# Kernel tuning notes

Hardware: AMD Instinct MI355X
Metric: run time of the kernel (lower is better)

Reference implementation:

```python
import jax, jax.numpy as jnp
import numpy as np

DIM = 1024
NUM_HEAD = 8
INNER = DIM // NUM_HEAD
B, L = 2, 2048
EPS = 1e-5  # GroupNorm default eps


def _xavier(key, out_d, in_d, gain=0.01):
    std = gain * np.sqrt(2.0 / (in_d + out_d))
    return (jax.random.normal(key, (out_d, in_d), jnp.float32) * std)


def setup_inputs() -> dict:
    key = jax.random.key(0)
    ks = jax.random.split(key, 12)
    x = jax.random.normal(ks[0], (B, L, DIM), jnp.float32)
    hidden = jax.random.normal(ks[1], (B, NUM_HEAD, INNER), jnp.float32)
    # dt bias: inv-softplus of dt ~ LogUniform(0.001, 0.1), as in __init__
    dt = jnp.exp(jax.random.uniform(ks[2], (NUM_HEAD,), jnp.float32,
                                    minval=np.log(0.001), maxval=np.log(0.1)))
    b_dt = dt + jnp.log1p(-jnp.exp(-dt))
    ln_a = jnp.log(jax.random.uniform(ks[3], (NUM_HEAD,), jnp.float32, minval=1.0, maxval=16.0))
    return {
        "x": x, "hidden": hidden,
        "W_z": _xavier(ks[4], DIM, DIM), "b_z": jnp.zeros((DIM,), jnp.float32),
        "W_z_act": _xavier(ks[5], DIM, DIM), "b_z_act": jnp.zeros((DIM,), jnp.float32),
        "W_y": _xavier(ks[6], DIM, DIM), "b_y": jnp.zeros((DIM,), jnp.float32),
        "W_y_act": _xavier(ks[7], DIM, DIM), "b_y_act": jnp.zeros((DIM,), jnp.float32),
        "W_dt": _xavier(ks[8], NUM_HEAD, DIM), "b_dt": b_dt,
        "ln_a": ln_a,
        "gn_w": jnp.ones((NUM_HEAD,), jnp.float32), "gn_b": jnp.zeros((NUM_HEAD,), jnp.float32),
    }


def reference(x, hidden, W_z, b_z, W_z_act, b_z_act, W_y, b_y, W_y_act, b_y_act,
              W_dt, b_dt, ln_a, gn_w, gn_b):
    b, l, d = x.shape
    nh, inner = NUM_HEAD, d // NUM_HEAD
    silu = jax.nn.silu
    xf = x.astype(jnp.float32)
    # gated input projection -> z: [b,l,h,i]
    z = ((xf @ W_z.T + b_z) * silu(xf @ W_z_act.T + b_z_act)).reshape(b, l, nh, inner)
    # log-decay per step: [b,l,h]
    ln_da = -jnp.exp(ln_a) * jax.nn.softplus(xf @ W_dt.T + b_dt)
    # einops.repeat 'b l h -> b l m h' then torch .tril(-1) (masks over LAST TWO dims (m,h))
    ln_da_masked = jnp.tril(jnp.broadcast_to(ln_da[:, :, None, :], (b, l, l, nh)), k=-1)
    # rfft/irfft conv with ones == prefix sum along l (dim 1)
    ln_da_masked_conv = jnp.cumsum(ln_da_masked, axis=1)
    da_masked_conv = jnp.tril(jnp.exp(ln_da_masked_conv))  # tril over (m,h), k=0
    h_inner = jnp.einsum('blmh,bmhi->blhi', da_masked_conv, z)
    # cross-chunk: cumulative decay applied to carried hidden state
    da_cum = jnp.exp(jnp.cumsum(ln_da, axis=1))  # [b,l,h]
    h_cross = jnp.einsum('blh,bhi->blhi', da_cum, hidden)
    h = h_inner + h_cross  # [b,l,h,i]
    hidden_next = h[:, -1]
    # GroupNorm(num_head groups, num_head channels) on [b*l, h, i]:
    # one channel per group -> normalize over inner dim per (token, head)
    mean = h.mean(axis=-1, keepdims=True)
    var = h.var(axis=-1, keepdims=True)
    h_norm = (h - mean) / jnp.sqrt(var + EPS) * gn_w[None, None, :, None] + gn_b[None, None, :, None]
    h_norm = h_norm.reshape(b, l, d)
    y = (h_norm @ W_y.T + b_y) * silu(xf @ W_y_act.T + b_y_act)
    return y.astype(x.dtype), hidden_next
```

## Files before the change

kernel.cpp:

```cpp
#include <hip/hip_runtime.h>
#include <stdint.h>

#define DIM   1024
#define L_SEQ 2048
#define BATCH 2
#define NH    8
#define M_TOT 4096
#define EPS_F 1e-5f

typedef __bf16 bf16x8 __attribute__((ext_vector_type(8)));
typedef unsigned short u16x8 __attribute__((ext_vector_type(8)));
typedef float f32x4 __attribute__((ext_vector_type(4)));

__device__ __forceinline__ unsigned short f2bf(float f) {
  unsigned int u = __float_as_uint(f);
  u += 0x7FFFu + ((u >> 16) & 1u);
  return (unsigned short)(u >> 16);
}

__device__ __forceinline__ f32x4 mfma_bf16(u16x8 a, u16x8 b, f32x4 c) {
  return __builtin_amdgcn_mfma_f32_16x16x32_bf16(
      __builtin_bit_cast(bf16x8, a), __builtin_bit_cast(bf16x8, b), c, 0, 0, 0);
}

__device__ __forceinline__ float silu_f(float v) {
  return v / (1.f + __expf(-v));
}

__device__ __forceinline__ void gload16(const unsigned short* g, unsigned short* l) {
  __builtin_amdgcn_global_load_lds(
      (const __attribute__((address_space(1))) unsigned int*)g,
      (__attribute__((address_space(3))) unsigned int*)l, 16, 0, 0);
}

__global__ __launch_bounds__(256) void prep_kernel(const float* __restrict__ x,
                                                   const float* __restrict__ W_dt,
                                                   const float* __restrict__ b_dt,
                                                   const float* __restrict__ ln_a,
                                                   const float4* __restrict__ wz,
                                                   const float4* __restrict__ wza,
                                                   const float4* __restrict__ wya,
                                                   float* __restrict__ ln_da,
                                                   unsigned short* __restrict__ xb,
                                                   ushort4* __restrict__ wzb,
                                                   ushort4* __restrict__ wzab,
                                                   ushort4* __restrict__ wyab,
                                                   float* __restrict__ Zs) {
  const int blk = blockIdx.x;
  const int tid = threadIdx.x;
  if (blk >= 4096) {
    const int wb = blk - 4096;
    if (wb < 2) ((f32x4*)Zs)[wb * 256 + tid] = f32x4{0.f, 0.f, 0.f, 0.f};
    int i = wb * 256 + tid;
    const float4* s; ushort4* d; int j;
    if (i < 262144)      { s = wz;  d = wzb;  j = i; }
    else if (i < 524288) { s = wza; d = wzab; j = i - 262144; }
    else                 { s = wya; d = wyab; j = i - 524288; }
    float4 f = s[j];
    d[j] = make_ushort4(f2bf(f.x), f2bf(f.y), f2bf(f.z), f2bf(f.w));
    return;
  }
  __shared__ float partials[NH][4];
  const int row = blk;
  const int wave = tid >> 6, lane = tid & 63;
  float4 f = ((const float4*)(x + (size_t)row * DIM))[tid];
  ((ushort4*)(xb + (size_t)row * DIM))[tid] =
      make_ushort4(f2bf(f.x), f2bf(f.y), f2bf(f.z), f2bf(f.w));
#pragma unroll
  for (int h = 0; h < NH; ++h) {
    const float4 w = ((const float4*)(W_dt + (size_t)h * DIM))[tid];
    float p = f.x * w.x + f.y * w.y + f.z * w.z + f.w * w.w;
    for (int off = 32; off > 0; off >>= 1) p += __shfl_down(p, off);
    if (lane == 0) partials[h][wave] = p;
  }
  __syncthreads();
  if (tid < 32) {
    const int h = tid >> 2, wv = tid & 3;
    float s = partials[h][wv];
    s += __shfl_down(s, 1);
    s += __shfl_down(s, 2);
    if (wv == 0) {
      float t = s + b_dt[h];
      float sp = (t > 20.f) ? t : log1pf(expf(t));
      int b = row >> 11, l = row & (L_SEQ - 1);
      ln_da[(size_t)(b * NH + h) * L_SEQ + l] = -expf(ln_a[h]) * sp;
    }
  }
}

__global__ __launch_bounds__(256, 4) void gemm_all(const unsigned short* __restrict__ xb,
                                                   const unsigned short* __restrict__ Wz,
                                                   const unsigned short* __restrict__ Wza,
                                                   const unsigned short* __restrict__ Wya,
                                                   const float* __restrict__ b_z,
                                                   const float* __restrict__ b_za,
                                                   const float* __restrict__ b_ya,
                                                   float* __restrict__ Zs,
                                                   float* __restrict__ wdiag,
                                                   float* __restrict__ Sy) {
  __shared__ __align__(16) unsigned short As[128 * 64];
  __shared__ __align__(16) unsigned short Bs[128 * 64];
  __shared__ float colsum[64];

  const int tid = threadIdx.x;
  const int lane = tid & 63, wave = tid >> 6;
  const int wm = wave >> 1, wn = wave & 1;
  const int l16 = lane & 15, quad = lane >> 4;

  const int flat = blockIdx.x;
  const int xcd = flat & 7;
  const int j = flat >> 3;
  const int nt = 3 * xcd + (j % 3);
  const int mt = j / 3;
  const bool isZ = (nt < 16);
  const int n0 = isZ ? nt * 64 : (nt - 16) * 128;
  const int m0 = mt * 128;

  const int rowl = tid >> 3;
  const int g = (tid & 7) ^ (rowl & 7);
  const size_t aoff = (size_t)(m0 + rowl) * DIM + g * 8;
  const size_t boff = (size_t)(n0 + rowl) * DIM + g * 8;
  const unsigned short* bp0 = isZ ? Wz : Wya;
  const unsigned short* bp1 = isZ ? Wza : (Wya + (size_t)64 * DIM);
  unsigned short* AsD = As + tid * 8;
  unsigned short* BsD = Bs + tid * 8;

  f32x4 acc[4][4];
  const f32x4 zero = {0.f, 0.f, 0.f, 0.f};
  for (int i = 0; i < 4; ++i)
    for (int jj = 0; jj < 4; ++jj) acc[i][jj] = zero;

  for (int kt = 0; kt < 16; ++kt) {
    const size_t k0 = (size_t)kt * 64;
    __syncthreads();
    gload16(xb  + aoff + k0,                AsD);
    gload16(xb  + aoff + 32 * DIM + k0,     AsD + 2048);
    gload16(xb  + aoff + 64 * DIM + k0,     AsD + 4096);
    gload16(xb  + aoff + 96 * DIM + k0,     AsD + 6144);
    gload16(bp0 + boff + k0,                BsD);
    gload16(bp0 + boff + 32 * DIM + k0,     BsD + 2048);
    gload16(bp1 + boff + k0,                BsD + 4096);
    gload16(bp1 + boff + 32 * DIM + k0,     BsD + 6144);
    __syncthreads();
#pragma unroll
    for (int kk = 0; kk < 2; ++kk) {
      const int kc = kk * 4 + quad;
      u16x8 aF[4], bF[4];
#pragma unroll
      for (int rb = 0; rb < 4; ++rb) {
        const int r = wm * 64 + rb * 16 + l16;
        aF[rb] = *(const u16x8*)&As[r * 64 + ((kc ^ (r & 7)) << 3)];
      }
#pragma unroll
      for (int cb = 0; cb < 4; ++cb) {
        int r;
        if (isZ) r = (cb < 2) ? (wn * 32 + cb * 16 + l16)
                              : (64 + wn * 32 + (cb - 2) * 16 + l16);
        else     r = wn * 64 + cb * 16 + l16;
        bF[cb] = *(const u16x8*)&Bs[r * 64 + ((kc ^ (r & 7)) << 3)];
      }
#pragma unroll
      for (int rb = 0; rb < 4; ++rb)
#pragma unroll
        for (int cb = 0; cb < 4; ++cb)
          acc[rb][cb] = mfma_bf16(aF[rb], bF[cb], acc[rb][cb]);
    }
  }

  if (isZ) {
    __syncthreads();
    if (tid < 64) colsum[tid] = 0.f;
    __syncthreads();
    const int b = m0 >> 11;
#pragma unroll
    for (int cb = 0; cb < 2; ++cb) {
      const int nl = wn * 32 + cb * 16 + l16;
      const int n = n0 + nl;
      const int h = n >> 7;
      const float bz = b_z[n], ba = b_za[n];
      float ssum = 0.f;
#pragma unroll
      for (int rb = 0; rb < 4; ++rb) {
        const int mlb = wm * 64 + rb * 16 + quad * 4;
#pragma unroll
        for (int r = 0; r < 4; ++r) {
          const int l = (m0 + mlb + r) & (L_SEQ - 1);
          float u  = acc[rb][cb][r] + bz;
          float vv = acc[rb][cb + 2][r] + ba;
          if (l > h) ssum += u * silu_f(vv);
          else if (l == h)
            wdiag[(size_t)(b * NH + h) * 128 + (n & 127)] = u * silu_f(vv);
        }
      }
      atomicAdd(&colsum[nl], ssum);
    }
    __syncthreads();
    if (tid < 64) atomicAdd(&Zs[(size_t)b * DIM + n0 + tid], colsum[tid]);
  } else {
#pragma unroll
    for (int cb = 0; cb < 4; ++cb) {
      const int nl = wn * 64 + cb * 16 + l16;
      const float bb = b_ya[n0 + nl];
#pragma unroll
      for (int rb = 0; rb < 4; ++rb) {
        const int mlb = wm * 64 + rb * 16 + quad * 4;
#pragma unroll
        for (int r = 0; r < 4; ++r)
          Sy[(size_t)(m0 + mlb + r) * DIM + n0 + nl] = silu_f(acc[rb][cb][r] + bb);
      }
    }
  }
}

__global__ __launch_bounds__(256) void stats_scan(const float* __restrict__ Zs,
                                                  const float* __restrict__ hidden,
                                                  const float* __restrict__ wdiag,
                                                  const float* __restrict__ gn_w,
                                                  const float* __restrict__ ln_da,
                                                  float* __restrict__ vtg,
                                                  float* __restrict__ wtg,
                                                  float* __restrict__ alpha2,
                                                  float* __restrict__ hidden_next) {
  const int bh = blockIdx.x, b = bh >> 3, h = bh & 7;
  const int tid = threadIdx.x, wv = tid >> 6, lane = tid & 63;
  __shared__ float csumS[32];
  __shared__ float statS[4];

  float v0 = 0.f, v1 = 0.f, w0 = 0.f, w1 = 0.f;
  const size_t base = (size_t)bh * 128;
  if (wv == 0) {
    v0 = Zs[(size_t)b * DIM + h * 128 + lane]      + hidden[base + lane];
    v1 = Zs[(size_t)b * DIM + h * 128 + 64 + lane] + hidden[base + 64 + lane];
    w0 = wdiag[base + lane];
    w1 = wdiag[base + 64 + lane];
    float sv = v0 + v1, sw = w0 + w1;
    for (int off = 32; off > 0; off >>= 1) {
      sv += __shfl_down(sv, off);
      sw += __shfl_down(sw, off);
    }
    const float muv = __shfl(sv, 0) * (1.f / 128.f);
    const float muw = __shfl(sw, 0) * (1.f / 128.f);
    const float a0 = v0 - muv, a1 = v1 - muv;
    const float c0 = w0 - muw, c1 = w1 - muw;
    float rvv = a0 * a0 + a1 * a1;
    float rvw = a0 * c0 + a1 * c1;
    float rww = c0 * c0 + c1 * c1;
    for (int off = 32; off > 0; off >>= 1) {
      rvv += __shfl_down(rvv, off);
      rvw += __shfl_down(rvw, off);
      rww += __shfl_down(rww, off);
    }
    if (lane == 0) {
      statS[0] = rvv * (1.f / 128.f);
      statS[1] = rvw * (1.f / 128.f);
      statS[2] = rww * (1.f / 128.f);
    }
    const float gw = gn_w[h];
    vtg[base + lane] = a0 * gw;  vtg[base + 64 + lane] = a1 * gw;
    wtg[base + lane] = c0 * gw;  wtg[base + 64 + lane] = c1 * gw;
  }

  const float* src = ln_da + (size_t)bh * L_SEQ;
  float vals[8];
#pragma unroll
  for (int jj = 0; jj < 8; ++jj) {
    const int c = wv * 8 + jj;
    float val = src[c * 64 + lane];
#pragma unroll
    for (int off = 1; off < 64; off <<= 1) {
      float nv = __shfl_up(val, off);
      if (lane >= off) val += nv;
    }
    vals[jj] = val;
    if (lane == 63) csumS[c] = val;
  }
  __syncthreads();

  if (tid < 32) {
    float s = csumS[tid];
    float incl = s;
#pragma unroll
    for (int off = 1; off < 32; off <<= 1) {
      float nv = __shfl_up(incl, off);
      if (tid >= off) incl += nv;
    }
    csumS[tid] = incl - s;
    if (tid == 31) statS[3] = incl;
  }
  __syncthreads();

  const float svv = statS[0], svw = statS[1], sww = statS[2];
#pragma unroll
  for (int jj = 0; jj < 8; ++jj) {
    const int c = wv * 8 + jj;
    const float S = csumS[c] + vals[jj];
    const float ce = expf(S);
    const float D = rsqrtf(ce * ce * svv + 2.f * ce * svw + sww + EPS_F);
    const int l = c * 64 + lane;
    float* ap = alpha2 + ((size_t)(b * L_SEQ + l) * NH + h) * 2;
    ap[0] = ce * D;
    ap[1] = D;
  }
  if (wv == 0) {
    const float clast = expf(statS[3]);
    hidden_next[base + lane]      = clast * v0 + w0;
    hidden_next[base + 64 + lane] = clast * v1 + w1;
  }
}

__global__ __launch_bounds__(256) void proj_kernel(const float* __restrict__ W_y,
                                                   const float* __restrict__ vtg,
                                                   const float* __restrict__ wtg,
                                                   const float* __restrict__ gn_b,
                                                   const float* __restrict__ b_y,
                                                   float* __restrict__ Gv,
                                                   float* __restrict__ Gw,
                                                   float* __restrict__ constc) {
  const int tid = threadIdx.x, wave = tid >> 6, lane = tid & 63;
  const int n = blockIdx.x * 4 + wave;
  const float4* row = (const float4*)(W_y + (size_t)n * DIM);
  const int half = lane >> 5, l32 = lane & 31;
  float cc = 0.f;
#pragma unroll
  for (int p = 0; p < 4; ++p) {
    const int h = p * 2 + half;
    float4 wv = row[p * 64 + lane];
    const float4 va = *(const float4*)&vtg[(size_t)h * 128 + l32 * 4];
    const float4 vb = *(const float4*)&vtg[(size_t)(8 + h) * 128 + l32 * 4];
    const float4 wa = *(const float4*)&wtg[(size_t)h * 128 + l32 * 4];
    const float4 wb = *(const float4*)&wtg[(size_t)(8 + h) * 128 + l32 * 4];
    float gv0 = wv.x * va.x + wv.y * va.y + wv.z * va.z + wv.w * va.w;
    float gv1 = wv.x * vb.x + wv.y * vb.y + wv.z * vb.z + wv.w * vb.w;
    float gw0 = wv.x * wa.x + wv.y * wa.y + wv.z * wa.z + wv.w * wa.w;
    float gw1 = wv.x * wb.x + wv.y * wb.y + wv.z * wb.z + wv.w * wb.w;
    cc += (wv.x + wv.y + wv.z + wv.w) * gn_b[h];
#pragma unroll
    for (int off = 16; off > 0; off >>= 1) {
      gv0 += __shfl_down(gv0, off, 32);
      gv1 += __shfl_down(gv1, off, 32);
      gw0 += __shfl_down(gw0, off, 32);
      gw1 += __shfl_down(gw1, off, 32);
    }
    if (l32 == 0) {
      Gv[(size_t)h * DIM + n]       = gv0;
      Gv[(size_t)(8 + h) * DIM + n] = gv1;
      Gw[(size_t)h * DIM + n]       = gw0;
      Gw[(size_t)(8 + h) * DIM + n] = gw1;
    }
  }
  for (int off = 32; off > 0; off >>= 1) cc += __shfl_down(cc, off);
  if (lane == 0) constc[n] = b_y[n] + cc;
}

__global__ __launch_bounds__(256) void finalize(const float* __restrict__ alpha2,
                                                const float* __restrict__ Gv,
                                                const float* __restrict__ Gw,
                                                const float* __restrict__ constc,
                                                float* __restrict__ y) {
  const int tid = threadIdx.x;
  const int n0 = blockIdx.x * 256;
  const int m0 = blockIdx.y * 64;
  const int b = m0 >> 11;
  __shared__ float aS[64 * 16];
  ((float4*)aS)[tid] = ((const float4*)(alpha2 + (size_t)m0 * 16))[tid];
  __syncthreads();
  const int c = tid & 63;
  const int rg = tid >> 6;
  const int n = n0 + c * 4;
  f32x4 g[16 * 2];
#pragma unroll
  for (int h = 0; h < 8; ++h) {
    g[2 * h]     = *(const f32x4*)&Gv[(size_t)(b * NH + h) * DIM + n];
    g[2 * h + 1] = *(const f32x4*)&Gw[(size_t)(b * NH + h) * DIM + n];
  }
  const f32x4 cc = *(const f32x4*)&constc[n];
#pragma unroll
  for (int jj = 0; jj < 16; ++jj) {
    const int m = m0 + rg * 16 + jj;
    const float* a = &aS[(rg * 16 + jj) * 16];
    f32x4 Ay = cc;
#pragma unroll
    for (int k = 0; k < 16; ++k) Ay += a[k] * g[k];
    f32x4 s = *(const f32x4*)&y[(size_t)m * DIM + n];
    *(f32x4*)&y[(size_t)m * DIM + n] = Ay * s;
  }
}

extern "C" void kernel_launch(void* const* d_in, const int* in_sizes, int n_in,
                              void* d_out, int out_size, void* d_ws, size_t ws_size,
                              hipStream_t stream) {
  const float* x      = (const float*)d_in[0];
  const float* hidden = (const float*)d_in[1];
  const float* W_z    = (const float*)d_in[2];
  const float* b_z    = (const float*)d_in[3];
  const float* W_za   = (const float*)d_in[4];
  const float* b_za   = (const float*)d_in[5];
  const float* W_y    = (const float*)d_in[6];
  const float* b_y    = (const float*)d_in[7];
  const float* W_ya   = (const float*)d_in[8];
  const float* b_ya   = (const float*)d_in[9];
  const float* W_dt   = (const float*)d_in[10];
  const float* b_dt   = (const float*)d_in[11];
  const float* ln_a   = (const float*)d_in[12];
  const float* gn_w   = (const float*)d_in[13];
  const float* gn_b   = (const float*)d_in[14];

  char* ws = (char*)d_ws;
  unsigned short* xb   = (unsigned short*)(ws);
  unsigned short* Wzb  = (unsigned short*)(ws + 8388608);
  unsigned short* Wzab = (unsigned short*)(ws + 10485760);
  unsigned short* Wyab = (unsigned short*)(ws + 12582912);
  float* ln_da  = (float*)(ws + 14680064);
  float* Zs     = (float*)(ws + 14811136);
  float* wdiag  = (float*)(ws + 14819328);
  float* vtg    = (float*)(ws + 14827520);
  float* wtg    = (float*)(ws + 14835712);
  float* Gv     = (float*)(ws + 14843904);
  float* Gw     = (float*)(ws + 14909440);
  float* constc = (float*)(ws + 14974976);
  float* alpha2 = (float*)(ws + 14979072);

  float* y = (float*)d_out;
  float* hidden_next = y + (size_t)M_TOT * DIM;

  prep_kernel<<<7168, 256, 0, stream>>>(x, W_dt, b_dt, ln_a,
                                        (const float4*)W_z, (const float4*)W_za,
                                        (const float4*)W_ya,
                                        ln_da, xb, (ushort4*)Wzb, (ushort4*)Wzab,
                                        (ushort4*)Wyab, Zs);

  gemm_all<<<768, 256, 0, stream>>>(xb, Wzb, Wzab, Wyab,
                                    b_z, b_za, b_ya, Zs, wdiag, y);

  stats_scan<<<16, 256, 0, stream>>>(Zs, hidden, wdiag, gn_w, ln_da,
                                     vtg, wtg, alpha2, hidden_next);
  proj_kernel<<<256, 256, 0, stream>>>(W_y, vtg, wtg, gn_b, b_y, Gv, Gw, constc);

  finalize<<<dim3(4, 64), 256, 0, stream>>>(alpha2, Gv, Gw, constc, y);
}
```

Before: 165.0 us.

## Merge five kernel launches into two persistent kernels with grid barriers

```diff
diff --git a/kernel.cpp b/kernel.cpp
--- a/kernel.cpp
+++ b/kernel.cpp
@@ -33,356 +33,387 @@
       (__attribute__((address_space(3))) unsigned int*)l, 16, 0, 0);
 }
 
-__global__ __launch_bounds__(256) void prep_kernel(const float* __restrict__ x,
-                                                   const float* __restrict__ W_dt,
-                                                   const float* __restrict__ b_dt,
-                                                   const float* __restrict__ ln_a,
-                                                   const float4* __restrict__ wz,
-                                                   const float4* __restrict__ wza,
-                                                   const float4* __restrict__ wya,
-                                                   float* __restrict__ ln_da,
-                                                   unsigned short* __restrict__ xb,
-                                                   ushort4* __restrict__ wzb,
-                                                   ushort4* __restrict__ wzab,
-                                                   ushort4* __restrict__ wyab,
-                                                   float* __restrict__ Zs) {
-  const int blk = blockIdx.x;
-  const int tid = threadIdx.x;
-  if (blk >= 4096) {
-    const int wb = blk - 4096;
-    if (wb < 2) ((f32x4*)Zs)[wb * 256 + tid] = f32x4{0.f, 0.f, 0.f, 0.f};
-    int i = wb * 256 + tid;
-    const float4* s; ushort4* d; int j;
-    if (i < 262144)      { s = wz;  d = wzb;  j = i; }
-    else if (i < 524288) { s = wza; d = wzab; j = i - 262144; }
-    else                 { s = wya; d = wyab; j = i - 524288; }
-    float4 f = s[j];
-    d[j] = make_ushort4(f2bf(f.x), f2bf(f.y), f2bf(f.z), f2bf(f.w));
-    return;
-  }
-  __shared__ float partials[NH][4];
-  const int row = blk;
-  const int wave = tid >> 6, lane = tid & 63;
-  float4 f = ((const float4*)(x + (size_t)row * DIM))[tid];
-  ((ushort4*)(xb + (size_t)row * DIM))[tid] =
-      make_ushort4(f2bf(f.x), f2bf(f.y), f2bf(f.z), f2bf(f.w));
-#pragma unroll
-  for (int h = 0; h < NH; ++h) {
-    const float4 w = ((const float4*)(W_dt + (size_t)h * DIM))[tid];
-    float p = f.x * w.x + f.y * w.y + f.z * w.z + f.w * w.w;
-    for (int off = 32; off > 0; off >>= 1) p += __shfl_down(p, off);
-    if (lane == 0) partials[h][wave] = p;
-  }
+
+__device__ __forceinline__ void grid_bar(unsigned int* cnt, unsigned int target) {
   __syncthreads();
-  if (tid < 32) {
-    const int h = tid >> 2, wv = tid & 3;
-    float s = partials[h][wv];
-    s += __shfl_down(s, 1);
-    s += __shfl_down(s, 2);
-    if (wv == 0) {
-      float t = s + b_dt[h];
-      float sp = (t > 20.f) ? t : log1pf(expf(t));
-      int b = row >> 11, l = row & (L_SEQ - 1);
-      ln_da[(size_t)(b * NH + h) * L_SEQ + l] = -expf(ln_a[h]) * sp;
-    }
-  }
-}
-
-__global__ __launch_bounds__(256, 4) void gemm_all(const unsigned short* __restrict__ xb,
-                                                   const unsigned short* __restrict__ Wz,
-                                                   const unsigned short* __restrict__ Wza,
-                                                   const unsigned short* __restrict__ Wya,
-                                                   const float* __restrict__ b_z,
-                                                   const float* __restrict__ b_za,
-                                                   const float* __restrict__ b_ya,
-                                                   float* __restrict__ Zs,
-                                                   float* __restrict__ wdiag,
-                                                   float* __restrict__ Sy) {
+  if (threadIdx.x == 0) {
+    __threadfence();
+    __hip_atomic_fetch_add(cnt, 1u, __ATOMIC_RELAXED, __HIP_MEMORY_SCOPE_AGENT);
+    while (__hip_atomic_load(cnt, __ATOMIC_RELAXED, __HIP_MEMORY_SCOPE_AGENT) < target) {
+      __builtin_amdgcn_s_sleep(8);
+    }
+    __threadfence();
+  }
+  __syncthreads();
+}
+
+__global__ __launch_bounds__(256, 4) void coop_main(
+    const float*  __restrict__ x,
+    const float*  __restrict__ W_dt,
+    const float*  __restrict__ b_dt,
+    const float*  __restrict__ ln_a,
+    const float4* __restrict__ wz4,
+    const float4* __restrict__ wza4,
+    const float4* __restrict__ wya4,
+    float*        __restrict__ ln_da,
+    unsigned short* __restrict__ xb,
+    float*        __restrict__ Zs,
+    const float*  __restrict__ b_z,
+    const float*  __restrict__ b_za,
+    const float*  __restrict__ b_ya,
+    float*        __restrict__ wdiag,
+    float*        __restrict__ y,
+    unsigned short* __restrict__ Wzb,
+    unsigned short* __restrict__ Wzab,
+    unsigned short* __restrict__ Wyab,
+    unsigned int*  __restrict__ bars) {
   __shared__ __align__(16) unsigned short As[128 * 64];
   __shared__ __align__(16) unsigned short Bs[128 * 64];
   __shared__ float colsum[64];
+  __shared__ float partials[NH][4];
 
   const int tid = threadIdx.x;
+  const int blk = blockIdx.x;
   const int lane = tid & 63, wave = tid >> 6;
-  const int wm = wave >> 1, wn = wave & 1;
-  const int l16 = lane & 15, quad = lane >> 4;
-
-  const int flat = blockIdx.x;
-  const int xcd = flat & 7;
-  const int j = flat >> 3;
-  const int nt = 3 * xcd + (j % 3);
-  const int mt = j / 3;
-  const bool isZ = (nt < 16);
-  const int n0 = isZ ? nt * 64 : (nt - 16) * 128;
-  const int m0 = mt * 128;
-
-  const int rowl = tid >> 3;
-  const int g = (tid & 7) ^ (rowl & 7);
-  const size_t aoff = (size_t)(m0 + rowl) * DIM + g * 8;
-  const size_t boff = (size_t)(n0 + rowl) * DIM + g * 8;
-  const unsigned short* bp0 = isZ ? Wz : Wya;
-  const unsigned short* bp1 = isZ ? Wza : (Wya + (size_t)64 * DIM);
-  unsigned short* AsD = As + tid * 8;
-  unsigned short* BsD = Bs + tid * 8;
-
-  f32x4 acc[4][4];
-  const f32x4 zero = {0.f, 0.f, 0.f, 0.f};
-  for (int i = 0; i < 4; ++i)
-    for (int jj = 0; jj < 4; ++jj) acc[i][jj] = zero;
-
-  for (int kt = 0; kt < 16; ++kt) {
-    const size_t k0 = (size_t)kt * 64;
-    __syncthreads();
-    gload16(xb  + aoff + k0,                AsD);
-    gload16(xb  + aoff + 32 * DIM + k0,     AsD + 2048);
-    gload16(xb  + aoff + 64 * DIM + k0,     AsD + 4096);
-    gload16(xb  + aoff + 96 * DIM + k0,     AsD + 6144);
-    gload16(bp0 + boff + k0,                BsD);
-    gload16(bp0 + boff + 32 * DIM + k0,     BsD + 2048);
-    gload16(bp1 + boff + k0,                BsD + 4096);
-    gload16(bp1 + boff + 32 * DIM + k0,     BsD + 6144);
-    __syncthreads();
-#pragma unroll
-    for (int kk = 0; kk < 2; ++kk) {
-      const int kc = kk * 4 + quad;
-      u16x8 aF[4], bF[4];
-#pragma unroll
-      for (int rb = 0; rb < 4; ++rb) {
-        const int r = wm * 64 + rb * 16 + l16;
-        aF[rb] = *(const u16x8*)&As[r * 64 + ((kc ^ (r & 7)) << 3)];
-      }
+
+  {
+    ushort4* wzb4  = (ushort4*)Wzb;
+    ushort4* wzab4 = (ushort4*)Wzab;
+    ushort4* wyab4 = (ushort4*)Wyab;
+#pragma unroll
+    for (int it = 0; it < 4; ++it) {
+      const int i = it * 196608 + blk * 256 + tid;
+      const float4* s; ushort4* d; int j;
+      if (i < 262144)      { s = wz4;  d = wzb4;  j = i; }
+      else if (i < 524288) { s = wza4; d = wzab4; j = i - 262144; }
+      else                 { s = wya4; d = wyab4; j = i - 524288; }
+      float4 f = s[j];
+      d[j] = make_ushort4(f2bf(f.x), f2bf(f.y), f2bf(f.z), f2bf(f.w));
+    }
+    if (blk == 0) {
+      ((f32x4*)Zs)[tid]       = f32x4{0.f, 0.f, 0.f, 0.f};
+      ((f32x4*)Zs)[tid + 256] = f32x4{0.f, 0.f, 0.f, 0.f};
+    }
+    for (int it = 0; it < 6; ++it) {
+      const int row = it * 768 + blk;
+      if (row < 4096) {
+        float4 f = ((const float4*)(x + (size_t)row * DIM))[tid];
+        ((ushort4*)(xb + (size_t)row * DIM))[tid] =
+            make_ushort4(f2bf(f.x), f2bf(f.y), f2bf(f.z), f2bf(f.w));
+#pragma unroll
+        for (int h = 0; h < NH; ++h) {
+          const float4 w = ((const float4*)(W_dt + (size_t)h * DIM))[tid];
+          float p = f.x * w.x + f.y * w.y + f.z * w.z + f.w * w.w;
+          for (int off = 32; off > 0; off >>= 1) p += __shfl_down(p, off);
+          if (lane == 0) partials[h][wave] = p;
+        }
+        __syncthreads();
+        if (tid < 32) {
+          const int h = tid >> 2, wv = tid & 3;
+          float s = partials[h][wv];
+          s += __shfl_down(s, 1);
+          s += __shfl_down(s, 2);
+          if (wv == 0) {
+            float t = s + b_dt[h];
+            float sp = (t > 20.f) ? t : log1pf(expf(t));
+            int b = row >> 11, l = row & (L_SEQ - 1);
+            ln_da[(size_t)(b * NH + h) * L_SEQ + l] = -expf(ln_a[h]) * sp;
+          }
+        }
+        __syncthreads();
+      }
+    }
+  }
+
+  grid_bar(bars + 0, 768u);
+
+  {
+    const int wm = wave >> 1, wn = wave & 1;
+    const int l16 = lane & 15, quad = lane >> 4;
+
+    const int flat = blk;
+    const int xcd = flat & 7;
+    const int j = flat >> 3;
+    const int nt = 3 * xcd + (j % 3);
+    const int mt = j / 3;
+    const bool isZ = (nt < 16);
+    const int n0 = isZ ? nt * 64 : (nt - 16) * 128;
+    const int m0 = mt * 128;
+
+    const int rowl = tid >> 3;
+    const int g = (tid & 7) ^ (rowl & 7);
+    const size_t aoff = (size_t)(m0 + rowl) * DIM + g * 8;
+    const size_t boff = (size_t)(n0 + rowl) * DIM + g * 8;
+    const unsigned short* bp0 = isZ ? Wzb : Wyab;
+    const unsigned short* bp1 = isZ ? Wzab : (Wyab + (size_t)64 * DIM);
+    unsigned short* AsD = As + tid * 8;
+    unsigned short* BsD = Bs + tid * 8;
+
+    f32x4 acc[4][4];
+    const f32x4 zero = {0.f, 0.f, 0.f, 0.f};
+    for (int i = 0; i < 4; ++i)
+      for (int jj = 0; jj < 4; ++jj) acc[i][jj] = zero;
+
+    for (int kt = 0; kt < 16; ++kt) {
+      const size_t k0 = (size_t)kt * 64;
+      __syncthreads();
+      gload16(xb  + aoff + k0,                AsD);
+      gload16(xb  + aoff + 32 * DIM + k0,     AsD + 2048);
+      gload16(xb  + aoff + 64 * DIM + k0,     AsD + 4096);
+      gload16(xb  + aoff + 96 * DIM + k0,     AsD + 6144);
+      gload16(bp0 + boff + k0,                BsD);
+      gload16(bp0 + boff + 32 * DIM + k0,     BsD + 2048);
+      gload16(bp1 + boff + k0,                BsD + 4096);
+      gload16(bp1 + boff + 32 * DIM + k0,     BsD + 6144);
+      __syncthreads();
+#pragma unroll
+      for (int kk = 0; kk < 2; ++kk) {
+        const int kc = kk * 4 + quad;
+        u16x8 aF[4], bF[4];
+#pragma unroll
+        for (int rb = 0; rb < 4; ++rb) {
+          const int r = wm * 64 + rb * 16 + l16;
+          aF[rb] = *(const u16x8*)&As[r * 64 + ((kc ^ (r & 7)) << 3)];
+        }
+#pragma unroll
+        for (int cb = 0; cb < 4; ++cb) {
+          int r;
+          if (isZ) r = (cb < 2) ? (wn * 32 + cb * 16 + l16)
+                                : (64 + wn * 32 + (cb - 2) * 16 + l16);
+          else     r = wn * 64 + cb * 16 + l16;
+          bF[cb] = *(const u16x8*)&Bs[r * 64 + ((kc ^ (r & 7)) << 3)];
+        }
+#pragma unroll
+        for (int rb = 0; rb < 4; ++rb)
+#pragma unroll
+          for (int cb = 0; cb < 4; ++cb)
+            acc[rb][cb] = mfma_bf16(aF[rb], bF[cb], acc[rb][cb]);
+      }
+    }
+
+    if (isZ) {
+      __syncthreads();
+      if (tid < 64) colsum[tid] = 0.f;
+      __syncthreads();
+      const int b = m0 >> 11;
+#pragma unroll
+      for (int cb = 0; cb < 2; ++cb) {
+        const int nl = wn * 32 + cb * 16 + l16;
+        const int n = n0 + nl;
+        const int h = n >> 7;
+        const float bz = b_z[n], ba = b_za[n];
+        float ssum = 0.f;
+#pragma unroll
+        for (int rb = 0; rb < 4; ++rb) {
+          const int mlb = wm * 64 + rb * 16 + quad * 4;
+#pragma unroll
+          for (int r = 0; r < 4; ++r) {
+            const int l = (m0 + mlb + r) & (L_SEQ - 1);
+            float u  = acc[rb][cb][r] + bz;
+            float vv = acc[rb][cb + 2][r] + ba;
+            if (l > h) ssum += u * silu_f(vv);
+            else if (l == h)
+              wdiag[(size_t)(b * NH + h) * 128 + (n & 127)] = u * silu_f(vv);
+          }
+        }
+        atomicAdd(&colsum[nl], ssum);
+      }
+      __syncthreads();
+      if (tid < 64) atomicAdd(&Zs[(size_t)b * DIM + n0 + tid], colsum[tid]);
+    } else {
 #pragma unroll
       for (int cb = 0; cb < 4; ++cb) {
-        int r;
-        if (isZ) r = (cb < 2) ? (wn * 32 + cb * 16 + l16)
-                              : (64 + wn * 32 + (cb - 2) * 16 + l16);
-        else     r = wn * 64 + cb * 16 + l16;
-        bF[cb] = *(const u16x8*)&Bs[r * 64 + ((kc ^ (r & 7)) << 3)];
-      }
-#pragma unroll
-      for (int rb = 0; rb < 4; ++rb)
-#pragma unroll
-        for (int cb = 0; cb < 4; ++cb)
-          acc[rb][cb] = mfma_bf16(aF[rb], bF[cb], acc[rb][cb]);
-    }
-  }
-
-  if (isZ) {
-    __syncthreads();
-    if (tid < 64) colsum[tid] = 0.f;
-    __syncthreads();
-    const int b = m0 >> 11;
-#pragma unroll
-    for (int cb = 0; cb < 2; ++cb) {
-      const int nl = wn * 32 + cb * 16 + l16;
-      const int n = n0 + nl;
-      const int h = n >> 7;
-      const float bz = b_z[n], ba = b_za[n];
-      float ssum = 0.f;
-#pragma unroll
-      for (int rb = 0; rb < 4; ++rb) {
-        const int mlb = wm * 64 + rb * 16 + quad * 4;
-#pragma unroll
-        for (int r = 0; r < 4; ++r) {
-          const int l = (m0 + mlb + r) & (L_SEQ - 1);
-          float u  = acc[rb][cb][r] + bz;
-          float vv = acc[rb][cb + 2][r] + ba;
-          if (l > h) ssum += u * silu_f(vv);
-          else if (l == h)
-            wdiag[(size_t)(b * NH + h) * 128 + (n & 127)] = u * silu_f(vv);
-        }
-      }
-      atomicAdd(&colsum[nl], ssum);
-    }
-    __syncthreads();
-    if (tid < 64) atomicAdd(&Zs[(size_t)b * DIM + n0 + tid], colsum[tid]);
-  } else {
-#pragma unroll
-    for (int cb = 0; cb < 4; ++cb) {
-      const int nl = wn * 64 + cb * 16 + l16;
-      const float bb = b_ya[n0 + nl];
-#pragma unroll
-      for (int rb = 0; rb < 4; ++rb) {
-        const int mlb = wm * 64 + rb * 16 + quad * 4;
-#pragma unroll
-        for (int r = 0; r < 4; ++r)
-          Sy[(size_t)(m0 + mlb + r) * DIM + n0 + nl] = silu_f(acc[rb][cb][r] + bb);
-      }
-    }
-  }
-}
-
-__global__ __launch_bounds__(256) void stats_scan(const float* __restrict__ Zs,
-                                                  const float* __restrict__ hidden,
-                                                  const float* __restrict__ wdiag,
-                                                  const float* __restrict__ gn_w,
-                                                  const float* __restrict__ ln_da,
-                                                  float* __restrict__ vtg,
-                                                  float* __restrict__ wtg,
-                                                  float* __restrict__ alpha2,
-                                                  float* __restrict__ hidden_next) {
-  const int bh = blockIdx.x, b = bh >> 3, h = bh & 7;
-  const int tid = threadIdx.x, wv = tid >> 6, lane = tid & 63;
+        const int nl = wn * 64 + cb * 16 + l16;
+        const float bb = b_ya[n0 + nl];
+#pragma unroll
+        for (int rb = 0; rb < 4; ++rb) {
+          const int mlb = wm * 64 + rb * 16 + quad * 4;
+#pragma unroll
+          for (int r = 0; r < 4; ++r)
+            y[(size_t)(m0 + mlb + r) * DIM + n0 + nl] = silu_f(acc[rb][cb][r] + bb);
+        }
+      }
+    }
+  }
+}
+
+__global__ __launch_bounds__(256) void coop_tail(
+    const float* __restrict__ Zs,
+    const float* __restrict__ hidden,
+    const float* __restrict__ wdiag,
+    const float* __restrict__ gn_w,
+    const float* __restrict__ ln_da,
+    float* __restrict__ vtg,
+    float* __restrict__ wtg,
+    float* __restrict__ alpha2,
+    float* __restrict__ hidden_next,
+    const float* __restrict__ W_y,
+    const float* __restrict__ gn_b,
+    const float* __restrict__ b_y,
+    float* __restrict__ Gv,
+    float* __restrict__ Gw,
+    float* __restrict__ constc,
+    float* __restrict__ y,
+    unsigned int* __restrict__ bars) {
+  const int tid = threadIdx.x;
+  const int blk = blockIdx.x;
   __shared__ float csumS[32];
   __shared__ float statS[4];
-
-  float v0 = 0.f, v1 = 0.f, w0 = 0.f, w1 = 0.f;
-  const size_t base = (size_t)bh * 128;
-  if (wv == 0) {
-    v0 = Zs[(size_t)b * DIM + h * 128 + lane]      + hidden[base + lane];
-    v1 = Zs[(size_t)b * DIM + h * 128 + 64 + lane] + hidden[base + 64 + lane];
-    w0 = wdiag[base + lane];
-    w1 = wdiag[base + 64 + lane];
-    float sv = v0 + v1, sw = w0 + w1;
-    for (int off = 32; off > 0; off >>= 1) {
-      sv += __shfl_down(sv, off);
-      sw += __shfl_down(sw, off);
-    }
-    const float muv = __shfl(sv, 0) * (1.f / 128.f);
-    const float muw = __shfl(sw, 0) * (1.f / 128.f);
-    const float a0 = v0 - muv, a1 = v1 - muv;
-    const float c0 = w0 - muw, c1 = w1 - muw;
-    float rvv = a0 * a0 + a1 * a1;
-    float rvw = a0 * c0 + a1 * c1;
-    float rww = c0 * c0 + c1 * c1;
-    for (int off = 32; off > 0; off >>= 1) {
-      rvv += __shfl_down(rvv, off);
-      rvw += __shfl_down(rvw, off);
-      rww += __shfl_down(rww, off);
-    }
-    if (lane == 0) {
-      statS[0] = rvv * (1.f / 128.f);
-      statS[1] = rvw * (1.f / 128.f);
-      statS[2] = rww * (1.f / 128.f);
-    }
-    const float gw = gn_w[h];
-    vtg[base + lane] = a0 * gw;  vtg[base + 64 + lane] = a1 * gw;
-    wtg[base + lane] = c0 * gw;  wtg[base + 64 + lane] = c1 * gw;
-  }
-
-  const float* src = ln_da + (size_t)bh * L_SEQ;
-  float vals[8];
-#pragma unroll
-  for (int jj = 0; jj < 8; ++jj) {
-    const int c = wv * 8 + jj;
-    float val = src[c * 64 + lane];
-#pragma unroll
-    for (int off = 1; off < 64; off <<= 1) {
-      float nv = __shfl_up(val, off);
-      if (lane >= off) val += nv;
-    }
-    vals[jj] = val;
-    if (lane == 63) csumS[c] = val;
-  }
-  __syncthreads();
-
-  if (tid < 32) {
-    float s = csumS[tid];
-    float incl = s;
-#pragma unroll
-    for (int off = 1; off < 32; off <<= 1) {
-      float nv = __shfl_up(incl, off);
-      if (tid >= off) incl += nv;
-    }
-    csumS[tid] = incl - s;
-    if (tid == 31) statS[3] = incl;
-  }
-  __syncthreads();
-
-  const float svv = statS[0], svw = statS[1], sww = statS[2];
-#pragma unroll
-  for (int jj = 0; jj < 8; ++jj) {
-    const int c = wv * 8 + jj;
-    const float S = csumS[c] + vals[jj];
-    const float ce = expf(S);
-    const float D = rsqrtf(ce * ce * svv + 2.f * ce * svw + sww + EPS_F);
-    const int l = c * 64 + lane;
-    float* ap = alpha2 + ((size_t)(b * L_SEQ + l) * NH + h) * 2;
-    ap[0] = ce * D;
-    ap[1] = D;
-  }
-  if (wv == 0) {
-    const float clast = expf(statS[3]);
-    hidden_next[base + lane]      = clast * v0 + w0;
-    hidden_next[base + 64 + lane] = clast * v1 + w1;
-  }
-}
-
-__global__ __launch_bounds__(256) void proj_kernel(const float* __restrict__ W_y,
-                                                   const float* __restrict__ vtg,
-                                                   const float* __restrict__ wtg,
-                                                   const float* __restrict__ gn_b,
-                                                   const float* __restrict__ b_y,
-                                                   float* __restrict__ Gv,
-                                                   float* __restrict__ Gw,
-                                                   float* __restrict__ constc) {
-  const int tid = threadIdx.x, wave = tid >> 6, lane = tid & 63;
-  const int n = blockIdx.x * 4 + wave;
-  const float4* row = (const float4*)(W_y + (size_t)n * DIM);
-  const int half = lane >> 5, l32 = lane & 31;
-  float cc = 0.f;
-#pragma unroll
-  for (int p = 0; p < 4; ++p) {
-    const int h = p * 2 + half;
-    float4 wv = row[p * 64 + lane];
-    const float4 va = *(const float4*)&vtg[(size_t)h * 128 + l32 * 4];
-    const float4 vb = *(const float4*)&vtg[(size_t)(8 + h) * 128 + l32 * 4];
-    const float4 wa = *(const float4*)&wtg[(size_t)h * 128 + l32 * 4];
-    const float4 wb = *(const float4*)&wtg[(size_t)(8 + h) * 128 + l32 * 4];
-    float gv0 = wv.x * va.x + wv.y * va.y + wv.z * va.z + wv.w * va.w;
-    float gv1 = wv.x * vb.x + wv.y * vb.y + wv.z * vb.z + wv.w * vb.w;
-    float gw0 = wv.x * wa.x + wv.y * wa.y + wv.z * wa.z + wv.w * wa.w;
-    float gw1 = wv.x * wb.x + wv.y * wb.y + wv.z * wb.z + wv.w * wb.w;
-    cc += (wv.x + wv.y + wv.z + wv.w) * gn_b[h];
-#pragma unroll
-    for (int off = 16; off > 0; off >>= 1) {
-      gv0 += __shfl_down(gv0, off, 32);
-      gv1 += __shfl_down(gv1, off, 32);
-      gw0 += __shfl_down(gw0, off, 32);
-      gw1 += __shfl_down(gw1, off, 32);
-    }
-    if (l32 == 0) {
-      Gv[(size_t)h * DIM + n]       = gv0;
-      Gv[(size_t)(8 + h) * DIM + n] = gv1;
-      Gw[(size_t)h * DIM + n]       = gw0;
-      Gw[(size_t)(8 + h) * DIM + n] = gw1;
-    }
-  }
-  for (int off = 32; off > 0; off >>= 1) cc += __shfl_down(cc, off);
-  if (lane == 0) constc[n] = b_y[n] + cc;
-}
-
-__global__ __launch_bounds__(256) void finalize(const float* __restrict__ alpha2,
-                                                const float* __restrict__ Gv,
-                                                const float* __restrict__ Gw,
-                                                const float* __restrict__ constc,
-                                                float* __restrict__ y) {
-  const int tid = threadIdx.x;
-  const int n0 = blockIdx.x * 256;
-  const int m0 = blockIdx.y * 64;
-  const int b = m0 >> 11;
   __shared__ float aS[64 * 16];
-  ((float4*)aS)[tid] = ((const float4*)(alpha2 + (size_t)m0 * 16))[tid];
-  __syncthreads();
-  const int c = tid & 63;
-  const int rg = tid >> 6;
-  const int n = n0 + c * 4;
-  f32x4 g[16 * 2];
-#pragma unroll
-  for (int h = 0; h < 8; ++h) {
-    g[2 * h]     = *(const f32x4*)&Gv[(size_t)(b * NH + h) * DIM + n];
-    g[2 * h + 1] = *(const f32x4*)&Gw[(size_t)(b * NH + h) * DIM + n];
-  }
-  const f32x4 cc = *(const f32x4*)&constc[n];
-#pragma unroll
-  for (int jj = 0; jj < 16; ++jj) {
-    const int m = m0 + rg * 16 + jj;
-    const float* a = &aS[(rg * 16 + jj) * 16];
-    f32x4 Ay = cc;
-#pragma unroll
-    for (int k = 0; k < 16; ++k) Ay += a[k] * g[k];
-    f32x4 s = *(const f32x4*)&y[(size_t)m * DIM + n];
-    *(f32x4*)&y[(size_t)m * DIM + n] = Ay * s;
+
+  if (blk < 16) {
+    const int bh = blk, b = bh >> 3, h = bh & 7;
+    const int wv = tid >> 6, lane = tid & 63;
+
+    float v0 = 0.f, v1 = 0.f, w0 = 0.f, w1 = 0.f;
+    const size_t base = (size_t)bh * 128;
+    if (wv == 0) {
+      v0 = Zs[(size_t)b * DIM + h * 128 + lane]      + hidden[base + lane];
+      v1 = Zs[(size_t)b * DIM + h * 128 + 64 + lane] + hidden[base + 64 + lane];
+      w0 = wdiag[base + lane];
+      w1 = wdiag[base + 64 + lane];
+      float sv = v0 + v1, sw = w0 + w1;
+      for (int off = 32; off > 0; off >>= 1) {
+        sv += __shfl_down(sv, off);
+        sw += __shfl_down(sw, off);
+      }
+      const float muv = __shfl(sv, 0) * (1.f / 128.f);
+      const float muw = __shfl(sw, 0) * (1.f / 128.f);
+      const float a0 = v0 - muv, a1 = v1 - muv;
+      const float c0 = w0 - muw, c1 = w1 - muw;
+      float rvv = a0 * a0 + a1 * a1;
+      float rvw = a0 * c0 + a1 * c1;
+      float rww = c0 * c0 + c1 * c1;
+      for (int off = 32; off > 0; off >>= 1) {
+        rvv += __shfl_down(rvv, off);
+        rvw += __shfl_down(rvw, off);
+        rww += __shfl_down(rww, off);
+      }
+      if (lane == 0) {
+        statS[0] = rvv * (1.f / 128.f);
+        statS[1] = rvw * (1.f / 128.f);
+        statS[2] = rww * (1.f / 128.f);
+      }
+      const float gw = gn_w[h];
+      vtg[base + lane] = a0 * gw;  vtg[base + 64 + lane] = a1 * gw;
+      wtg[base + lane] = c0 * gw;  wtg[base + 64 + lane] = c1 * gw;
+    }
+
+    const float* src = ln_da + (size_t)bh * L_SEQ;
+    float vals[8];
+#pragma unroll
+    for (int jj = 0; jj < 8; ++jj) {
+      const int c = wv * 8 + jj;
+      float val = src[c * 64 + lane];
+#pragma unroll
+      for (int off = 1; off < 64; off <<= 1) {
+        float nv = __shfl_up(val, off);
+        if (lane >= off) val += nv;
+      }
+      vals[jj] = val;
+      if (lane == 63) csumS[c] = val;
+    }
+    __syncthreads();
+
+    if (tid < 32) {
+      float s = csumS[tid];
+      float incl = s;
+#pragma unroll
+      for (int off = 1; off < 32; off <<= 1) {
+        float nv = __shfl_up(incl, off);
+        if (tid >= off) incl += nv;
+      }
+      csumS[tid] = incl - s;
+      if (tid == 31) statS[3] = incl;
+    }
+    __syncthreads();
+
+    const float svv = statS[0], svw = statS[1], sww = statS[2];
+#pragma unroll
+    for (int jj = 0; jj < 8; ++jj) {
+      const int c = wv * 8 + jj;
+      const float S = csumS[c] + vals[jj];
+      const float ce = expf(S);
+      const float D = rsqrtf(ce * ce * svv + 2.f * ce * svw + sww + EPS_F);
+      const int l = c * 64 + lane;
+      float* ap = alpha2 + ((size_t)(b * L_SEQ + l) * NH + h) * 2;
+      ap[0] = ce * D;
+      ap[1] = D;
+    }
+    if (wv == 0) {
+      const float clast = expf(statS[3]);
+      hidden_next[base + lane]      = clast * v0 + w0;
+      hidden_next[base + 64 + lane] = clast * v1 + w1;
+    }
+  }
+
+  grid_bar(bars + 1, 256u);
+
+  {
+    const int wave = tid >> 6, lane = tid & 63;
+    const int n = blk * 4 + wave;
+    const float4* row = (const float4*)(W_y + (size_t)n * DIM);
+    const int half = lane >> 5, l32 = lane & 31;
+    float cc = 0.f;
+#pragma unroll
+    for (int p = 0; p < 4; ++p) {
+      const int h = p * 2 + half;
+      float4 wv = row[p * 64 + lane];
+      const float4 va = *(const float4*)&vtg[(size_t)h * 128 + l32 * 4];
+      const float4 vb = *(const float4*)&vtg[(size_t)(8 + h) * 128 + l32 * 4];
+      const float4 wa = *(const float4*)&wtg[(size_t)h * 128 + l32 * 4];
+      const float4 wb = *(const float4*)&wtg[(size_t)(8 + h) * 128 + l32 * 4];
+      float gv0 = wv.x * va.x + wv.y * va.y + wv.z * va.z + wv.w * va.w;
+      float gv1 = wv.x * vb.x + wv.y * vb.y + wv.z * vb.z + wv.w * vb.w;
+      float gw0 = wv.x * wa.x + wv.y * wa.y + wv.z * wa.z + wv.w * wa.w;
+      float gw1 = wv.x * wb.x + wv.y * wb.y + wv.z * wb.z + wv.w * wb.w;
+      cc += (wv.x + wv.y + wv.z + wv.w) * gn_b[h];
+#pragma unroll
+      for (int off = 16; off > 0; off >>= 1) {
+        gv0 += __shfl_down(gv0, off, 32);
+        gv1 += __shfl_down(gv1, off, 32);
+        gw0 += __shfl_down(gw0, off, 32);
+        gw1 += __shfl_down(gw1, off, 32);
+      }
+      if (l32 == 0) {
+        Gv[(size_t)h * DIM + n]       = gv0;
+        Gv[(size_t)(8 + h) * DIM + n] = gv1;
+        Gw[(size_t)h * DIM + n]       = gw0;
+        Gw[(size_t)(8 + h) * DIM + n] = gw1;
+      }
+    }
+    for (int off = 32; off > 0; off >>= 1) cc += __shfl_down(cc, off);
+    if (lane == 0) constc[n] = b_y[n] + cc;
+  }
+
+  grid_bar(bars + 2, 256u);
+
+  {
+    const int n0 = (blk & 3) * 256;
+    const int m0 = (blk >> 2) * 64;
+    const int b = m0 >> 11;
+    ((float4*)aS)[tid] = ((const float4*)(alpha2 + (size_t)m0 * 16))[tid];
+    __syncthreads();
+    const int c = tid & 63;
+    const int rg = tid >> 6;
+    const int n = n0 + c * 4;
+    f32x4 g[16 * 2];
+#pragma unroll
+    for (int h = 0; h < 8; ++h) {
+      g[2 * h]     = *(const f32x4*)&Gv[(size_t)(b * NH + h) * DIM + n];
+      g[2 * h + 1] = *(const f32x4*)&Gw[(size_t)(b * NH + h) * DIM + n];
+    }
+    const f32x4 cc = *(const f32x4*)&constc[n];
+#pragma unroll
+    for (int jj = 0; jj < 16; ++jj) {
+      const int m = m0 + rg * 16 + jj;
+      const float* a = &aS[(rg * 16 + jj) * 16];
+      f32x4 Ay = cc;
+#pragma unroll
+      for (int k = 0; k < 16; ++k) Ay += a[k] * g[k];
+      f32x4 s = *(const f32x4*)&y[(size_t)m * DIM + n];
+      *(f32x4*)&y[(size_t)m * DIM + n] = Ay * s;
+    }
   }
 }
 
@@ -419,22 +450,20 @@
   float* Gw     = (float*)(ws + 14909440);
   float* constc = (float*)(ws + 14974976);
   float* alpha2 = (float*)(ws + 14979072);
+  unsigned int* bars = (unsigned int*)(ws + 15241216);
 
   float* y = (float*)d_out;
   float* hidden_next = y + (size_t)M_TOT * DIM;
 
-  prep_kernel<<<7168, 256, 0, stream>>>(x, W_dt, b_dt, ln_a,
-                                        (const float4*)W_z, (const float4*)W_za,
-                                        (const float4*)W_ya,
-                                        ln_da, xb, (ushort4*)Wzb, (ushort4*)Wzab,
-                                        (ushort4*)Wyab, Zs);
-
-  gemm_all<<<768, 256, 0, stream>>>(xb, Wzb, Wzab, Wyab,
-                                    b_z, b_za, b_ya, Zs, wdiag, y);
-
-  stats_scan<<<16, 256, 0, stream>>>(Zs, hidden, wdiag, gn_w, ln_da,
-                                     vtg, wtg, alpha2, hidden_next);
-  proj_kernel<<<256, 256, 0, stream>>>(W_y, vtg, wtg, gn_b, b_y, Gv, Gw, constc);
-
-  finalize<<<dim3(4, 64), 256, 0, stream>>>(alpha2, Gv, Gw, constc, y);
-}
+  hipMemsetAsync(bars, 0, 256, stream);
+
+  coop_main<<<768, 256, 0, stream>>>(x, W_dt, b_dt, ln_a,
+                                     (const float4*)W_z, (const float4*)W_za,
+                                     (const float4*)W_ya,
+                                     ln_da, xb, Zs, b_z, b_za, b_ya,
+                                     wdiag, y, Wzb, Wzab, Wyab, bars);
+
+  coop_tail<<<256, 256, 0, stream>>>(Zs, hidden, wdiag, gn_w, ln_da,
+                                     vtg, wtg, alpha2, hidden_next,
+                                     W_y, gn_b, b_y, Gv, Gw, constc, y, bars);
+}
```

Result: slower. 258.0 us (+56.3%).
